# Kernel optimization log

Measured on AMD Instinct MI355X. Metric: run time of the kernel, lower is better.

Reference implementation:

```python
import jax, jax.numpy as jnp
import numpy as np

B, I, O = 2048, 512, 512

def setup_inputs() -> dict:
    key = jax.random.key(0)
    kx, kw, ks = jax.random.split(key, 3)
    x = jax.random.uniform(kx, (B, I), dtype=jnp.float32)
    # shift weight logits so sigmoid(w) ~ 0.02: keeps the length-I product
    # of implication factors away from underflow (sparse conjunction)
    w_logits = jax.random.normal(kw, (I, O), dtype=jnp.float32) - 4.0
    s_logits = jax.random.normal(ks, (I, O), dtype=jnp.float32)
    return {"x": x, "w_logits": w_logits, "s_logits": s_logits}

def reference(x, w_logits, s_logits):
    # FuzzyParam.value(): sigmoid of stored logits
    w = jax.nn.sigmoid(w_logits)   # (I, O)
    s = jax.nn.sigmoid(s_logits)   # (I, O)
    xi = x[:, :, None]             # (B, I, 1)
    # product fuzzy logic:
    #   bin_xnor(a, b) = a*b + (1-a)*(1-b)
    #   implies(a, b)  = 1 - a*(1 - b)
    #   conjoin        = prod along axis
    xnor = xi * s + (1.0 - xi) * (1.0 - s)      # (B, I, O)
    factors = 1.0 - w * (1.0 - xnor)            # (B, I, O)
    return jnp.prod(factors, axis=1)            # (B, O)
```

## Files before the change

### kernel.cpp

```cpp
#include <hip/hip_runtime.h>
#include <hip/hip_bf16.h>
#include <math.h>

#define B_DIM 2048
#define I_DIM 512
#define O_DIM 512

constexpr int R_ROWS  = 8;
constexpr int W_CHUNK = 4;
constexpr int CHUNK   = I_DIM / W_CHUNK;
constexpr int KP      = CHUNK / 2;
constexpr int KROWS   = I_DIM / 2;

__global__ __launch_bounds__(256) void precompute_ab(
    const float* __restrict__ w_logits,
    const float* __restrict__ s_logits,
    float4* __restrict__ ab4)
{
    int t = blockIdx.x * 256 + threadIdx.x;
    int o  = t & (O_DIM - 1);
    int k  = t >> 9;
    int i0 = 2 * k;

    float zw0 = w_logits[(i0 + 0) * O_DIM + o];
    float zs0 = s_logits[(i0 + 0) * O_DIM + o];
    float zw1 = w_logits[(i0 + 1) * O_DIM + o];
    float zs1 = s_logits[(i0 + 1) * O_DIM + o];

    float w0 = 1.0f / (1.0f + expf(-zw0));
    float s0 = 1.0f / (1.0f + expf(-zs0));
    float w1 = 1.0f / (1.0f + expf(-zw1));
    float s1 = 1.0f / (1.0f + expf(-zs1));

    float4 v;
    v.x = fmaf(-w0, s0, 1.0f);
    v.y = fmaf(-w1, s1, 1.0f);
    v.z = w0 * (2.0f * s0 - 1.0f);
    v.w = w1 * (2.0f * s1 - 1.0f);
    ab4[k * O_DIM + o] = v;
}

__global__ __launch_bounds__(1024, 8) void fuzzy_main(
    const float* __restrict__ x,
    const float4* __restrict__ ab4,
    float* __restrict__ out)
{
    __shared__ float part[W_CHUNK][R_ROWS][256];

    const int o_l = threadIdx.x;
    const int o   = blockIdx.x * 256 + o_l;
    const int y   = __builtin_amdgcn_readfirstlane((int)threadIdx.y);
    const int b0  = blockIdx.y * R_ROWS;

    const float*  xp  = x + b0 * I_DIM + y * CHUNK;
    const int     kbase = y * KP;

    float acc0[R_ROWS], acc1[R_ROWS];
#pragma unroll
    for (int r = 0; r < R_ROWS; ++r) { acc0[r] = 1.0f; acc1[r] = 1.0f; }

    float4 p0 = ab4[(size_t)(kbase + 0) * O_DIM + o];
    float4 p1 = ab4[(size_t)(kbase + 1) * O_DIM + o];

    for (int k = 0; k < KP; k += 2) {
        float4 c0 = p0;
        float4 c1 = p1;
        int kn = (kbase + k + 2) & (KROWS - 1);
        p0 = ab4[(size_t)(kn + 0) * O_DIM + o];
        p1 = ab4[(size_t)(kn + 1) * O_DIM + o];

        const int i = 2 * k;
#pragma unroll
        for (int r = 0; r < R_ROWS; ++r) {
            const float* xr = xp + r * I_DIM + i;
            float x0 = xr[0];
            float x1 = xr[1];
            float x2 = xr[2];
            float x3 = xr[3];
            float f0 = fmaf(c0.z, x0, c0.x);
            float f1 = fmaf(c0.w, x1, c0.y);
            float f2 = fmaf(c1.z, x2, c1.x);
            float f3 = fmaf(c1.w, x3, c1.y);
            float h0 = f0 * f2;
            float h1 = f1 * f3;
            acc0[r] *= h0;
            acc1[r] *= h1;
        }
    }

#pragma unroll
    for (int r = 0; r < R_ROWS; ++r)
        part[y][r][o_l] = acc0[r] * acc1[r];
    __syncthreads();
#pragma unroll
    for (int rr = 0; rr < 2; ++rr) {
        int r8 = y * 2 + rr;
        float v = part[0][r8][o_l] * part[1][r8][o_l]
                * part[2][r8][o_l] * part[3][r8][o_l];
        out[(size_t)(b0 + r8) * O_DIM + o] = v;
    }
}

extern "C" void kernel_launch(void* const* d_in, const int* in_sizes, int n_in,
                              void* d_out, int out_size, void* d_ws, size_t ws_size,
                              hipStream_t stream) {
    const float* x        = (const float*)d_in[0];
    const float* w_logits = (const float*)d_in[1];
    const float* s_logits = (const float*)d_in[2];
    float* out = (float*)d_out;
    float4* ab4 = (float4*)d_ws;

    precompute_ab<<<dim3((I_DIM / 2) * O_DIM / 256), dim3(256), 0, stream>>>(
        w_logits, s_logits, ab4);

    fuzzy_main<<<dim3(O_DIM / 256, B_DIM / R_ROWS), dim3(256, W_CHUNK), 0, stream>>>(
        x, ab4, out);
}
```

Measured before the change: 94.40 us.

## Transpose x into row-interleaved quads and use packed FP32 FMA/MUL

Adds a pass in the setup kernel that rearranges x so that, for each group of 8 batch rows, the float4 quads of all rows sit contiguously, letting the main loop fetch each row's four x values with one 16-byte load. The inner loop switches to v_pk_fma_f32 and v_pk_mul_f32 through inline asm, which halves the VALU instruction count for the product chain. The cost is an extra 4 MB read and write of x in the setup kernel plus a larger workspace, and the inline asm may limit compiler scheduling.

```diff
diff --git a/kernel.cpp b/kernel.cpp
--- a/kernel.cpp
+++ b/kernel.cpp
@@ -11,37 +11,62 @@
 constexpr int CHUNK   = I_DIM / W_CHUNK;
 constexpr int KP      = CHUNK / 2;
 constexpr int KROWS   = I_DIM / 2;
+constexpr int QUADS   = I_DIM / 4;
 
-__global__ __launch_bounds__(256) void precompute_ab(
+typedef float v2f __attribute__((ext_vector_type(2)));
+
+static __device__ __forceinline__ v2f pk_fma(v2f a, v2f b, v2f c) {
+    v2f d;
+    asm("v_pk_fma_f32 %0, %1, %2, %3" : "=v"(d) : "v"(a), "v"(b), "v"(c));
+    return d;
+}
+static __device__ __forceinline__ v2f pk_mul(v2f a, v2f b) {
+    v2f d;
+    asm("v_pk_mul_f32 %0, %1, %2" : "=v"(d) : "v"(a), "v"(b));
+    return d;
+}
+
+__global__ __launch_bounds__(256) void setup_kernel(
+    const float* __restrict__ x,
     const float* __restrict__ w_logits,
     const float* __restrict__ s_logits,
-    float4* __restrict__ ab4)
+    float4* __restrict__ ab4,
+    float4* __restrict__ xt4)
 {
-    int t = blockIdx.x * 256 + threadIdx.x;
-    int o  = t & (O_DIM - 1);
-    int k  = t >> 9;
-    int i0 = 2 * k;
+    const int blk = blockIdx.x;
+    if (blk < 512) {
+        int t = blk * 256 + threadIdx.x;
+        int o  = t & (O_DIM - 1);
+        int k  = t >> 9;
+        int i0 = 2 * k;
 
-    float zw0 = w_logits[(i0 + 0) * O_DIM + o];
-    float zs0 = s_logits[(i0 + 0) * O_DIM + o];
-    float zw1 = w_logits[(i0 + 1) * O_DIM + o];
-    float zs1 = s_logits[(i0 + 1) * O_DIM + o];
+        float zw0 = w_logits[(i0 + 0) * O_DIM + o];
+        float zs0 = s_logits[(i0 + 0) * O_DIM + o];
+        float zw1 = w_logits[(i0 + 1) * O_DIM + o];
+        float zs1 = s_logits[(i0 + 1) * O_DIM + o];
 
-    float w0 = 1.0f / (1.0f + expf(-zw0));
-    float s0 = 1.0f / (1.0f + expf(-zs0));
-    float w1 = 1.0f / (1.0f + expf(-zw1));
-    float s1 = 1.0f / (1.0f + expf(-zs1));
+        float w0 = 1.0f / (1.0f + expf(-zw0));
+        float s0 = 1.0f / (1.0f + expf(-zs0));
+        float w1 = 1.0f / (1.0f + expf(-zw1));
+        float s1 = 1.0f / (1.0f + expf(-zs1));
 
-    float4 v;
-    v.x = fmaf(-w0, s0, 1.0f);
-    v.y = fmaf(-w1, s1, 1.0f);
-    v.z = w0 * (2.0f * s0 - 1.0f);
-    v.w = w1 * (2.0f * s1 - 1.0f);
-    ab4[k * O_DIM + o] = v;
+        float4 v;
+        v.x = fmaf(-w0, s0, 1.0f);
+        v.y = fmaf(-w1, s1, 1.0f);
+        v.z = w0 * (2.0f * s0 - 1.0f);
+        v.w = w1 * (2.0f * s1 - 1.0f);
+        ab4[k * O_DIM + o] = v;
+    } else {
+        int t  = (blk - 512) * 256 + threadIdx.x;
+        int q  = t & (QUADS - 1);
+        int b  = t >> 7;
+        float4 v = ((const float4*)x)[(size_t)b * QUADS + q];
+        xt4[((size_t)(b >> 3) * QUADS + q) * R_ROWS + (b & 7)] = v;
+    }
 }
 
 __global__ __launch_bounds__(1024, 8) void fuzzy_main(
-    const float* __restrict__ x,
+    const float* __restrict__ xt,
     const float4* __restrict__ ab4,
     float* __restrict__ out)
 {
@@ -50,14 +75,16 @@
     const int o_l = threadIdx.x;
     const int o   = blockIdx.x * 256 + o_l;
     const int y   = __builtin_amdgcn_readfirstlane((int)threadIdx.y);
-    const int b0  = blockIdx.y * R_ROWS;
+    const int g   = blockIdx.y;
+    const int b0  = g * R_ROWS;
+    const int kbase = y * KP;
 
-    const float*  xp  = x + b0 * I_DIM + y * CHUNK;
-    const int     kbase = y * KP;
+    const float4* xq = (const float4*)xt
+                     + ((size_t)g * QUADS + (size_t)y * (KP / 2)) * R_ROWS;
 
-    float acc0[R_ROWS], acc1[R_ROWS];
+    v2f acc[R_ROWS];
 #pragma unroll
-    for (int r = 0; r < R_ROWS; ++r) { acc0[r] = 1.0f; acc1[r] = 1.0f; }
+    for (int r = 0; r < R_ROWS; ++r) acc[r] = (v2f){1.0f, 1.0f};
 
     float4 p0 = ab4[(size_t)(kbase + 0) * O_DIM + o];
     float4 p1 = ab4[(size_t)(kbase + 1) * O_DIM + o];
@@ -69,28 +96,24 @@
         p0 = ab4[(size_t)(kn + 0) * O_DIM + o];
         p1 = ab4[(size_t)(kn + 1) * O_DIM + o];
 
-        const int i = 2 * k;
+        const v2f a01 = (v2f){c0.x, c0.y}, b01 = (v2f){c0.z, c0.w};
+        const v2f a23 = (v2f){c1.x, c1.y}, b23 = (v2f){c1.z, c1.w};
+
+        const float4* xrow = xq + (size_t)(k >> 1) * R_ROWS;
 #pragma unroll
         for (int r = 0; r < R_ROWS; ++r) {
-            const float* xr = xp + r * I_DIM + i;
-            float x0 = xr[0];
-            float x1 = xr[1];
-            float x2 = xr[2];
-            float x3 = xr[3];
-            float f0 = fmaf(c0.z, x0, c0.x);
-            float f1 = fmaf(c0.w, x1, c0.y);
-            float f2 = fmaf(c1.z, x2, c1.x);
-            float f3 = fmaf(c1.w, x3, c1.y);
-            float h0 = f0 * f2;
-            float h1 = f1 * f3;
-            acc0[r] *= h0;
-            acc1[r] *= h1;
+            float4 xv = xrow[r];
+            v2f x01 = (v2f){xv.x, xv.y};
+            v2f x23 = (v2f){xv.z, xv.w};
+            v2f f01 = pk_fma(b01, x01, a01);
+            v2f f23 = pk_fma(b23, x23, a23);
+            acc[r]  = pk_mul(acc[r], pk_mul(f01, f23));
         }
     }
 
 #pragma unroll
     for (int r = 0; r < R_ROWS; ++r)
-        part[y][r][o_l] = acc0[r] * acc1[r];
+        part[y][r][o_l] = acc[r].x * acc[r].y;
     __syncthreads();
 #pragma unroll
     for (int rr = 0; rr < 2; ++rr) {
@@ -109,10 +132,11 @@
     const float* s_logits = (const float*)d_in[2];
     float* out = (float*)d_out;
     float4* ab4 = (float4*)d_ws;
+    float4* xt4 = (float4*)((char*)d_ws + (size_t)I_DIM * O_DIM * 8);
 
-    precompute_ab<<<dim3((I_DIM / 2) * O_DIM / 256), dim3(256), 0, stream>>>(
-        w_logits, s_logits, ab4);
+    setup_kernel<<<dim3(1536), dim3(256), 0, stream>>>(
+        x, w_logits, s_logits, ab4, xt4);
 
     fuzzy_main<<<dim3(O_DIM / 256, B_DIM / R_ROWS), dim3(256, W_CHUNK), 0, stream>>>(
-        x, ab4, out);
+        (const float*)xt4, ab4, out);
 }
```

Result: slower. 103.2 us (+9.3%).
